# Performance work log

Measured on AMD Instinct MI355X. Metric: run time of the kernel, lower is better.

## Reference

```python
import jax, jax.numpy as jnp
import numpy as np

B, S, D, H = 2, 2048, 1024, 16  # batch, seq, rep_dim, num_heads
DH = D // H
MASK_VALUE = -1e-06  # value passed by MHAttention to masked_softmax (NOT -1e6)


def setup_inputs() -> dict:
    key = jax.random.key(0)
    ks = jax.random.split(key, 16)
    def xavier(k, shape):
        fan_in, fan_out = shape[0], shape[1]
        limit = float(np.sqrt(6.0 / (fan_in + fan_out)))
        return jax.random.uniform(k, shape, jnp.float32, -limit, limit)
    return {
        "queries": jax.random.normal(ks[0], (B, S, D), jnp.float32),
        "keys": jax.random.normal(ks[1], (B, S, D), jnp.float32),
        "values": jax.random.normal(ks[2], (B, S, D), jnp.float32),
        "thresholds": jax.random.randint(ks[3], (B,), 1, S + 1, jnp.int32),
        # Linear params stored as (in, out) so y = x @ W + b
        "Wq": xavier(ks[4], (D, D)), "bq": jnp.zeros((D,), jnp.float32),
        "Wk": xavier(ks[5], (D, D)), "bk": jnp.zeros((D,), jnp.float32),
        "Wv": xavier(ks[6], (D, D)), "bv": jnp.zeros((D,), jnp.float32),
        "W": xavier(ks[7], (DH, DH)),  # learnable bilinear attention matrix
        "Wo": xavier(ks[8], (D, D)), "bo": jnp.zeros((D,), jnp.float32),
    }


def reference(queries, keys, values, thresholds, Wq, bq, Wk, bk, Wv, bv, W, Wo, bo):
    def split_heads(x):  # (B,S,D) -> (B,H,S,DH)
        return x.reshape(B, S, H, DH).transpose(0, 2, 1, 3)

    Q = split_heads(queries @ Wq + bq)
    K = split_heads(keys @ Wk + bk)
    V = split_heads(values @ Wv + bv)

    # bilinear scores: (Q @ W) @ K^T, no 1/sqrt(d) scaling in original
    scores = jnp.einsum("bhqd,bhkd->bhqk", Q @ W, K)
    # mask key positions >= threshold[b] with MASK_VALUE before softmax
    keep = jnp.arange(S)[None, None, None, :] < thresholds[:, None, None, None]
    scores = jnp.where(keep, scores, MASK_VALUE)
    attn = jax.nn.softmax(scores, axis=-1)

    out = jnp.einsum("bhqk,bhkd->bhqd", attn, V)
    out = out.transpose(0, 2, 1, 3).reshape(B, S, D)  # merge heads
    return out @ Wo + bo
```

## Files before the change

### kernel.cpp

```cpp
#include <hip/hip_runtime.h>
#include <hip/hip_bf16.h>

#define D_MODEL 1024
#define NHEADS  16
#define DH      64
#define SEQ     2048
#define BATCH   2

#define LOG2E 1.4426950408889634f
#define MASKB2 (-1e-6f * LOG2E)
#define DEFER_THR 11.5456f
#define NEG_INF (-__builtin_inff())

typedef __attribute__((ext_vector_type(8))) short short8;
typedef __attribute__((ext_vector_type(4))) short short4v;
typedef __attribute__((ext_vector_type(4))) float f32x4;

#define AS1C(p) ((const __attribute__((address_space(1))) void*)(p))
#define AS3(p)  ((__attribute__((address_space(3))) void*)(p))

union PB { short4v s4; unsigned int u[2]; };

static __device__ __forceinline__ float fexp2(float x) {
    return __builtin_amdgcn_exp2f(x);
}

static __device__ __forceinline__ unsigned int pk2(float lo, float hi) {
    __hip_bfloat16 a = __float2bfloat16(lo), b = __float2bfloat16(hi);
    unsigned short au = *(unsigned short*)&a, bu = *(unsigned short*)&b;
    return (unsigned int)au | ((unsigned int)bu << 16);
}

__global__ __launch_bounds__(256) void fold_kernel(const float* __restrict__ Wq,
                                                   const float* __restrict__ bq,
                                                   const float* __restrict__ W,
                                                   float* __restrict__ Wq2,
                                                   float* __restrict__ bq2) {
    if (blockIdx.x < 4096) {
        int idx = blockIdx.x * 256 + threadIdx.x;
        int row = idx >> 10;
        int col = idx & 1023;
        int h = col >> 6, j = col & 63;
        const float* wqr = Wq + (size_t)row * D_MODEL + h * DH;
        float s = 0.f;
#pragma unroll
        for (int d = 0; d < DH; ++d) s += wqr[d] * W[d * DH + j];
        Wq2[idx] = s * LOG2E;
    } else {
        int col = (blockIdx.x - 4096) * 256 + threadIdx.x;
        int h = col >> 6, j = col & 63;
        float s = 0.f;
#pragma unroll
        for (int d = 0; d < DH; ++d) s += bq[h * DH + d] * W[d * DH + j];
        bq2[col] = s * LOG2E;
    }
}

__global__ __launch_bounds__(256) void convert3_kernel(const float* __restrict__ q,
                                                       const float* __restrict__ k,
                                                       const float* __restrict__ v,
                                                       __hip_bfloat16* __restrict__ oq,
                                                       __hip_bfloat16* __restrict__ ok,
                                                       __hip_bfloat16* __restrict__ ov) {
    int z = blockIdx.x >> 11;
    int i = (blockIdx.x & 2047) * 256 + threadIdx.x;
    const float* in = (z == 0) ? q : (z == 1) ? k : v;
    __hip_bfloat16* out = (z == 0) ? oq : (z == 1) ? ok : ov;
    float4 a = *(const float4*)(in + (size_t)i * 8);
    float4 b = *(const float4*)(in + (size_t)i * 8 + 4);
    __hip_bfloat16 o[8];
    o[0] = __float2bfloat16(a.x); o[1] = __float2bfloat16(a.y);
    o[2] = __float2bfloat16(a.z); o[3] = __float2bfloat16(a.w);
    o[4] = __float2bfloat16(b.x); o[5] = __float2bfloat16(b.y);
    o[6] = __float2bfloat16(b.z); o[7] = __float2bfloat16(b.w);
    *(short8*)(out + (size_t)i * 8) = *(short8*)o;
}

__global__ __launch_bounds__(256) void transpose4_kernel(const float* __restrict__ W0,
                                                         const float* __restrict__ W1,
                                                         const float* __restrict__ W2,
                                                         const float* __restrict__ W3,
                                                         __hip_bfloat16* __restrict__ T0,
                                                         __hip_bfloat16* __restrict__ T1,
                                                         __hip_bfloat16* __restrict__ T2,
                                                         __hip_bfloat16* __restrict__ T3) {
    __shared__ float sT[32][33];
    int z = blockIdx.z;
    const float* Win = (z == 0) ? W0 : (z == 1) ? W1 : (z == 2) ? W2 : W3;
    __hip_bfloat16* Wt = (z == 0) ? T0 : (z == 1) ? T1 : (z == 2) ? T2 : T3;
    int n0 = blockIdx.x * 32, k0 = blockIdx.y * 32;
    int tx = threadIdx.x & 31, ty = threadIdx.x >> 5;
#pragma unroll
    for (int i = 0; i < 4; ++i)
        sT[ty + i * 8][tx] = Win[(size_t)(k0 + ty + i * 8) * D_MODEL + n0 + tx];
    __syncthreads();
#pragma unroll
    for (int i = 0; i < 4; ++i)
        Wt[(size_t)(n0 + ty + i * 8) * D_MODEL + k0 + tx] = __float2bfloat16(sT[tx][ty + i * 8]);
}

#define GEMM_CORE(A_, BT_)                                                                  \
    __shared__ __hip_bfloat16 sA[2][128 * 32];                                              \
    __shared__ __hip_bfloat16 sB[2][128 * 32];                                              \
    const int t = threadIdx.x;                                                              \
    const int lane = t & 63, w = t >> 6;                                                    \
    const int g = lane >> 4, li = lane & 15;                                                \
    const int r0 = blockIdx.y * 128, c0 = blockIdx.x * 128;                                 \
    const int wr = (w >> 1) * 64, wc = (w & 1) * 64;                                        \
    f32x4 acc[4][4] = {};                                                                   \
    auto stage = [&](int bb, int k0) {                                                      \
        _Pragma("unroll")                                                                   \
        for (int i = 0; i < 2; ++i) {                                                       \
            int o = (i * 4 + w) * 1024 + lane * 16;                                         \
            int row = o >> 6, ce = (o & 63) >> 1;                                           \
            __builtin_amdgcn_global_load_lds(AS1C(A_ + (size_t)(r0 + row) * 1024 + k0 + ce),\
                                             AS3((char*)sA[bb] + (i * 4 + w) * 1024), 16, 0, 0); \
            __builtin_amdgcn_global_load_lds(AS1C(BT_ + (size_t)(c0 + row) * 1024 + k0 + ce),\
                                             AS3((char*)sB[bb] + (i * 4 + w) * 1024), 16, 0, 0); \
        }                                                                                   \
    };                                                                                      \
    stage(0, 0);                                                                            \
    asm volatile("s_waitcnt vmcnt(0)" ::: "memory");                                        \
    __syncthreads();                                                                        \
    int cur = 0;                                                                            \
    for (int k0 = 0; k0 < 1024; k0 += 32) {                                                 \
        if (k0 + 32 < 1024) stage(cur ^ 1, k0 + 32);                                        \
        short8 af[4], bf[4];                                                                \
        _Pragma("unroll")                                                                   \
        for (int m = 0; m < 4; ++m)                                                         \
            af[m] = *(const short8*)(sA[cur] + (wr + m * 16 + li) * 32 + g * 8);            \
        _Pragma("unroll")                                                                   \
        for (int n = 0; n < 4; ++n)                                                         \
            bf[n] = *(const short8*)(sB[cur] + (wc + n * 16 + li) * 32 + g * 8);            \
        _Pragma("unroll")                                                                   \
        for (int m = 0; m < 4; ++m)                                                         \
            _Pragma("unroll")                                                               \
            for (int n = 0; n < 4; ++n)                                                     \
                acc[m][n] = __builtin_amdgcn_mfma_f32_16x16x32_bf16(af[m], bf[n], acc[m][n], 0, 0, 0); \
        asm volatile("s_waitcnt vmcnt(0)" ::: "memory");                                    \
        __syncthreads();                                                                    \
        cur ^= 1;                                                                           \
    }

__global__ __launch_bounds__(256) void gemm_qkv_kernel(
    const __hip_bfloat16* __restrict__ Xq, const __hip_bfloat16* __restrict__ Xk,
    const __hip_bfloat16* __restrict__ Xv,
    const __hip_bfloat16* __restrict__ WqT, const __hip_bfloat16* __restrict__ WkT,
    const __hip_bfloat16* __restrict__ WvT,
    const float* __restrict__ bq2, const float* __restrict__ bk, const float* __restrict__ bv,
    __hip_bfloat16* __restrict__ Qp, __hip_bfloat16* __restrict__ Kp,
    __hip_bfloat16* __restrict__ Vt) {
    const int z = blockIdx.z;
    const __hip_bfloat16* A  = (z == 0) ? Xq  : (z == 1) ? Xk  : Xv;
    const __hip_bfloat16* BT = (z == 0) ? WqT : (z == 1) ? WkT : WvT;
    const float* bias        = (z == 0) ? bq2 : (z == 1) ? bk  : bv;
    __hip_bfloat16* C        = (z == 0) ? Qp  : (z == 1) ? Kp  : Vt;

    GEMM_CORE(A, BT)

#pragma unroll
    for (int m = 0; m < 4; ++m) {
#pragma unroll
        for (int n = 0; n < 4; ++n) {
            int col = c0 + wc + n * 16 + li;
            float bs = bias[col];
            int row0 = r0 + wr + m * 16 + g * 4;
            int h = col >> 6, d = col & 63;
            if (z == 2) {
                int b = row0 >> 11, s0 = row0 & 2047;
                __hip_bfloat16 o4[4];
#pragma unroll
                for (int r = 0; r < 4; ++r) o4[r] = __float2bfloat16(acc[m][n][r] + bs);
                *(short4*)(C + (((size_t)(b * NHEADS + h)) * DH + d) * SEQ + s0) = *(short4*)o4;
            } else {
#pragma unroll
                for (int r = 0; r < 4; ++r) {
                    int row = row0 + r;
                    int b = row >> 11, s = row & 2047;
                    C[(((size_t)(b * NHEADS + h)) * SEQ + s) * DH + d] =
                        __float2bfloat16(acc[m][n][r] + bs);
                }
            }
        }
    }
}

__global__ __launch_bounds__(256) void gemm_out_kernel(
    const __hip_bfloat16* __restrict__ A, const __hip_bfloat16* __restrict__ BT,
    const float* __restrict__ bias, float* __restrict__ C) {
    GEMM_CORE(A, BT)
#pragma unroll
    for (int m = 0; m < 4; ++m) {
#pragma unroll
        for (int n = 0; n < 4; ++n) {
            int col = c0 + wc + n * 16 + li;
            float bs = bias[col];
            int row0 = r0 + wr + m * 16 + g * 4;
#pragma unroll
            for (int r = 0; r < 4; ++r)
                C[(size_t)(row0 + r) * D_MODEL + col] = acc[m][n][r] + bs;
        }
    }
}

__global__ __launch_bounds__(256) void vsum_kernel(const __hip_bfloat16* __restrict__ Vt,
                                                   const int* __restrict__ thresholds,
                                                   float* __restrict__ Vsum) {
    int bh = blockIdx.x, b = bh >> 4;
    int thresh = thresholds[b];
    int loop_end = min(SEQ, ((thresh + 63) >> 6) << 6);
    int t = threadIdx.x;
    int dh = t >> 2, sub = t & 3;
    const __hip_bfloat16* row = Vt + ((size_t)bh * DH + dh) * SEQ;
    float s = 0.f;
    for (int s0 = loop_end + sub * 8; s0 < SEQ; s0 += 32) {
        short8 v = *(const short8*)(row + s0);
#pragma unroll
        for (int j = 0; j < 8; ++j) {
            unsigned short us = (unsigned short)v[j];
            s += __bfloat162float(*(__hip_bfloat16*)&us);
        }
    }
    s += __shfl_xor(s, 1);
    s += __shfl_xor(s, 2);
    if (sub == 0) Vsum[bh * DH + dh] = s;
}

__global__ __launch_bounds__(256) void attn_mfma_kernel(
    const __hip_bfloat16* __restrict__ Qp,
    const __hip_bfloat16* __restrict__ Kp,
    const __hip_bfloat16* __restrict__ Vt,
    const int* __restrict__ thresholds,
    const float* __restrict__ Vsum,
    __hip_bfloat16* __restrict__ AO) {
    __shared__ char lds[32768];
    char* sK  = lds;
    char* sVT = lds + 16384;

    const int t = threadIdx.x, lane = t & 63, w = t >> 6;
    const int g = lane >> 4, li = lane & 15;
    const int bh = blockIdx.x, b = bh >> 4, h = bh & 15;
    const int q0 = blockIdx.y * 64;
    const int thresh = thresholds[b];
    const int loop_end = min(SEQ, ((thresh + 63) >> 6) << 6);
    const __hip_bfloat16* Qb = Qp + (size_t)bh * SEQ * DH;
    const __hip_bfloat16* Kb = Kp + (size_t)bh * SEQ * DH;
    const __hip_bfloat16* Vb = Vt + (size_t)bh * DH * SEQ;

    short8 qf[2];
#pragma unroll
    for (int kb = 0; kb < 2; ++kb)
        qf[kb] = *(const short8*)(Qb + (size_t)(q0 + w * 16 + li) * DH + kb * 32 + g * 8);

    f32x4 Oacc[4] = {};
    float mrun = NEG_INF, lrun = 0.f;

    auto stageK = [&](int bb, int kv) {
#pragma unroll
        for (int i = 0; i < 2; ++i) {
            int o = i * 4096 + w * 1024 + lane * 16;
            int key = o >> 7, slot = (o & 127) >> 4;
            __builtin_amdgcn_global_load_lds(
                AS1C(Kb + (size_t)(kv + key) * DH + ((slot ^ (key & 7)) << 3)),
                AS3(sK + bb * 8192 + i * 4096 + w * 1024), 16, 0, 0);
        }
    };
    auto stageV = [&](int bb, int kv) {
#pragma unroll
        for (int i = 0; i < 2; ++i) {
            int o = i * 4096 + w * 1024 + lane * 16;
            int dh = o >> 7, slot = (o & 127) >> 4;
            __builtin_amdgcn_global_load_lds(
                AS1C(Vb + (size_t)dh * SEQ + kv + ((slot ^ (dh & 7)) << 3)),
                AS3(sVT + bb * 8192 + i * 4096 + w * 1024), 16, 0, 0);
        }
    };

    stageK(0, 0); stageV(0, 0);
    asm volatile("s_waitcnt vmcnt(0)" ::: "memory");
    __syncthreads();

    int cur = 0;
    for (int kv0 = 0; kv0 < loop_end; kv0 += 64) {
        int nxt = kv0 + 64;
        if (nxt < loop_end) { stageK(cur ^ 1, nxt); stageV(cur ^ 1, nxt); }

        f32x4 S[4] = {};
        __builtin_amdgcn_s_setprio(1);
#pragma unroll
        for (int kb = 0; kb < 2; ++kb) {
            short8 kf[4];
#pragma unroll
            for (int n = 0; n < 4; ++n) {
                int key = 16 * n + li;
                kf[n] = *(const short8*)(sK + cur * 8192 + key * 128 +
                                         (((4 * kb + g) ^ (key & 7)) << 4));
            }
#pragma unroll
            for (int n = 0; n < 4; ++n)
                S[n] = __builtin_amdgcn_mfma_f32_16x16x32_bf16(kf[n], qf[kb], S[n], 0, 0, 0);
        }
        __builtin_amdgcn_s_setprio(0);

        if (kv0 + 64 > thresh) {
            int tr = thresh - kv0 - 4 * g;
#pragma unroll
            for (int n = 0; n < 4; ++n)
#pragma unroll
                for (int rr = 0; rr < 4; ++rr)
                    if (16 * n + rr >= tr) S[n][rr] = MASKB2;
        }

        float mx = S[0][0];
#pragma unroll
        for (int n = 0; n < 4; ++n)
#pragma unroll
            for (int rr = 0; rr < 4; ++rr) mx = fmaxf(mx, S[n][rr]);
        mx = fmaxf(mx, __shfl_xor(mx, 16));
        mx = fmaxf(mx, __shfl_xor(mx, 32));
        float pmax = mx;

        if (__any(pmax > mrun + DEFER_THR)) {
            float mn = fmaxf(mrun, pmax);
            float alpha = fexp2(mrun - mn);
            lrun *= alpha;
#pragma unroll
            for (int n = 0; n < 4; ++n)
#pragma unroll
                for (int rr = 0; rr < 4; ++rr) Oacc[n][rr] *= alpha;
            mrun = mn;
        }

        short4v pb[4];
        float rs = 0.f;
#pragma unroll
        for (int n = 0; n < 4; ++n) {
#pragma unroll
            for (int rr = 0; rr < 4; ++rr) {
                float p = fexp2(S[n][rr] - mrun);
                S[n][rr] = p;
                rs += p;
            }
            PB u;
            u.u[0] = pk2(S[n][0], S[n][1]);
            u.u[1] = pk2(S[n][2], S[n][3]);
            pb[n] = u.s4;
        }
        rs += __shfl_xor(rs, 16);
        rs += __shfl_xor(rs, 32);
        lrun += rs;

        __builtin_amdgcn_s_setprio(1);
#pragma unroll
        for (int ks = 0; ks < 4; ++ks) {
            int slot = 2 * ks + (g >> 1);
            int sub8 = 8 * (g & 1);
#pragma unroll
            for (int n = 0; n < 4; ++n) {
                int dh = 16 * n + li;
                short4v va = *(const short4v*)(sVT + cur * 8192 + dh * 128 +
                                               ((slot ^ (dh & 7)) << 4) + sub8);
                Oacc[n] = __builtin_amdgcn_mfma_f32_16x16x16bf16_1k(va, pb[ks], Oacc[n], 0, 0, 0);
            }
        }
        __builtin_amdgcn_s_setprio(0);

        asm volatile("s_waitcnt vmcnt(0)" ::: "memory");
        __syncthreads();
        cur ^= 1;
    }

    int nmask = SEQ - loop_end;
    if (nmask > 0) {
        const float* vs = Vsum + bh * DH;
        f32x4 vsf[4];
#pragma unroll
        for (int n = 0; n < 4; ++n) vsf[n] = *(const f32x4*)(vs + 16 * n + 4 * g);
        float pu = fexp2(MASKB2 - mrun);
        lrun += (float)nmask * pu;
#pragma unroll
        for (int n = 0; n < 4; ++n)
#pragma unroll
            for (int rr = 0; rr < 4; ++rr) Oacc[n][rr] += pu * vsf[n][rr];
    }

    float linv = 1.0f / lrun;
    int q = q0 + w * 16 + li;
#pragma unroll
    for (int n = 0; n < 4; ++n) {
        __hip_bfloat16 o4[4];
#pragma unroll
        for (int rr = 0; rr < 4; ++rr) o4[rr] = __float2bfloat16(Oacc[n][rr] * linv);
        *(short4*)(AO + (size_t)(b * SEQ + q) * D_MODEL + h * DH + 16 * n + 4 * g) =
            *(short4*)o4;
    }
}

extern "C" void kernel_launch(void* const* d_in, const int* in_sizes, int n_in,
                              void* d_out, int out_size, void* d_ws, size_t ws_size,
                              hipStream_t stream) {
    const float* queries    = (const float*)d_in[0];
    const float* keys       = (const float*)d_in[1];
    const float* values     = (const float*)d_in[2];
    const int*   thresholds = (const int*)d_in[3];
    const float* Wq = (const float*)d_in[4];
    const float* bq = (const float*)d_in[5];
    const float* Wk = (const float*)d_in[6];
    const float* bk = (const float*)d_in[7];
    const float* Wv = (const float*)d_in[8];
    const float* bv = (const float*)d_in[9];
    const float* W  = (const float*)d_in[10];
    const float* Wo = (const float*)d_in[11];
    const float* bo = (const float*)d_in[12];
    float* out = (float*)d_out;

    char* wsb = (char*)d_ws;
    float* bq2  = (float*)wsb;
    float* Vsum = (float*)(wsb + 4096);
    float* Wq2  = (float*)(wsb + 16384);
    __hip_bfloat16* XqB = (__hip_bfloat16*)(wsb + 16384 + (4 << 20));
    __hip_bfloat16* XkB = XqB + (1 << 22);
    __hip_bfloat16* XvB = XkB + (1 << 22);
    __hip_bfloat16* WqT = XvB + (1 << 22);
    __hip_bfloat16* WkT = WqT + (1 << 20);
    __hip_bfloat16* WvT = WkT + (1 << 20);
    __hip_bfloat16* WoT = WvT + (1 << 20);
    __hip_bfloat16* QpB = WoT + (1 << 20);
    __hip_bfloat16* KpB = QpB + (1 << 22);
    __hip_bfloat16* VtB = KpB + (1 << 22);
    __hip_bfloat16* AOB = XqB;

    fold_kernel<<<4100, 256, 0, stream>>>(Wq, bq, W, Wq2, bq2);
    convert3_kernel<<<6144, 256, 0, stream>>>(queries, keys, values, XqB, XkB, XvB);
    transpose4_kernel<<<dim3(32, 32, 4), 256, 0, stream>>>(Wq2, Wk, Wv, Wo,
                                                           WqT, WkT, WvT, WoT);

    gemm_qkv_kernel<<<dim3(8, 32, 3), 256, 0, stream>>>(XqB, XkB, XvB, WqT, WkT, WvT,
                                                        bq2, bk, bv, QpB, KpB, VtB);
    vsum_kernel<<<32, 256, 0, stream>>>(VtB, thresholds, Vsum);

    attn_mfma_kernel<<<dim3(32, 32), 256, 0, stream>>>(QpB, KpB, VtB, thresholds, Vsum, AOB);

    gemm_out_kernel<<<dim3(8, 32), 256, 0, stream>>>(AOB, WoT, bo, out);
}
```

Baseline: 174.0 us.

## Fuse fp32-to-bf16 input conversion into QKV GEMM and software-pipeline attention

Removes the separate convert kernel. The QKV GEMM now loads fp32 activations directly into swizzled LDS and packs them to bf16 in registers, which saves a full write/read round trip of the converted inputs. The attention loop is also restructured into a two-stage software pipeline: the QK^T MFMAs and V fragment loads for tile t+1 are issued before the softmax and PV for tile t, so the two phases can overlap. The cost is twice the LDS for the A tile, extra conversion work inside the GEMM loop, and higher register pressure in attention from the doubled S and V register sets.

New measurement: 248.6 us. 42.9% more time.

```diff
diff --git a/kernel.cpp b/kernel.cpp
--- a/kernel.cpp
+++ b/kernel.cpp
@@ -19,7 +19,8 @@
 #define AS1C(p) ((const __attribute__((address_space(1))) void*)(p))
 #define AS3(p)  ((__attribute__((address_space(3))) void*)(p))
 
-union PB { short4v s4; unsigned int u[2]; };
+union PB  { short4v s4; unsigned int u[2]; };
+union PW8 { short8  s8; unsigned int u[4]; };
 
 static __device__ __forceinline__ float fexp2(float x) {
     return __builtin_amdgcn_exp2f(x);
@@ -54,26 +55,6 @@
         for (int d = 0; d < DH; ++d) s += bq[h * DH + d] * W[d * DH + j];
         bq2[col] = s * LOG2E;
     }
-}
-
-__global__ __launch_bounds__(256) void convert3_kernel(const float* __restrict__ q,
-                                                       const float* __restrict__ k,
-                                                       const float* __restrict__ v,
-                                                       __hip_bfloat16* __restrict__ oq,
-                                                       __hip_bfloat16* __restrict__ ok,
-                                                       __hip_bfloat16* __restrict__ ov) {
-    int z = blockIdx.x >> 11;
-    int i = (blockIdx.x & 2047) * 256 + threadIdx.x;
-    const float* in = (z == 0) ? q : (z == 1) ? k : v;
-    __hip_bfloat16* out = (z == 0) ? oq : (z == 1) ? ok : ov;
-    float4 a = *(const float4*)(in + (size_t)i * 8);
-    float4 b = *(const float4*)(in + (size_t)i * 8 + 4);
-    __hip_bfloat16 o[8];
-    o[0] = __float2bfloat16(a.x); o[1] = __float2bfloat16(a.y);
-    o[2] = __float2bfloat16(a.z); o[3] = __float2bfloat16(a.w);
-    o[4] = __float2bfloat16(b.x); o[5] = __float2bfloat16(b.y);
-    o[6] = __float2bfloat16(b.z); o[7] = __float2bfloat16(b.w);
-    *(short8*)(out + (size_t)i * 8) = *(short8*)o;
 }
 
 __global__ __launch_bounds__(256) void transpose4_kernel(const float* __restrict__ W0,
@@ -98,6 +79,66 @@
     for (int i = 0; i < 4; ++i)
         Wt[(size_t)(n0 + ty + i * 8) * D_MODEL + k0 + tx] = __float2bfloat16(sT[tx][ty + i * 8]);
 }
+
+#define GEMM_CORE_F32A(A_, BT_)                                                             \
+    __shared__ float sAf[2][128 * 32];                                                      \
+    __shared__ __hip_bfloat16 sB[2][128 * 32];                                              \
+    const int t = threadIdx.x;                                                              \
+    const int lane = t & 63, w = t >> 6;                                                    \
+    const int g = lane >> 4, li = lane & 15;                                                \
+    const int r0 = blockIdx.y * 128, c0 = blockIdx.x * 128;                                 \
+    const int wr = (w >> 1) * 64, wc = (w & 1) * 64;                                        \
+    f32x4 acc[4][4] = {};                                                                   \
+    auto stage = [&](int bb, int k0) {                                                      \
+        _Pragma("unroll")                                                                   \
+        for (int i = 0; i < 4; ++i) {                                                       \
+            int o = (i * 4 + w) * 1024 + lane * 16;              \
+            int row = o >> 7;                                                \
+            int slot = (o & 127) >> 4;                                                      \
+            int sslot = slot ^ (row & 7);                    \
+            __builtin_amdgcn_global_load_lds(                                               \
+                AS1C(A_ + (size_t)(r0 + row) * 1024 + k0 + sslot * 4),                      \
+                AS3((char*)sAf[bb] + (i * 4 + w) * 1024), 16, 0, 0);                        \
+        }                                                                                   \
+        _Pragma("unroll")                                                                   \
+        for (int i = 0; i < 2; ++i) {                                                       \
+            int o = (i * 4 + w) * 1024 + lane * 16;                                         \
+            int row = o >> 6, ce = (o & 63) >> 1;                                           \
+            __builtin_amdgcn_global_load_lds(AS1C(BT_ + (size_t)(c0 + row) * 1024 + k0 + ce),\
+                                             AS3((char*)sB[bb] + (i * 4 + w) * 1024), 16, 0, 0); \
+        }                                                                                   \
+    };                                                                                      \
+    stage(0, 0);                                                                            \
+    asm volatile("s_waitcnt vmcnt(0)" ::: "memory");                                        \
+    __syncthreads();                                                                        \
+    const int xr0 = (((2 * g)     ^ (li & 7)) << 4);                                        \
+    const int xr1 = (((2 * g + 1) ^ (li & 7)) << 4);                                        \
+    int cur = 0;                                                                            \
+    for (int k0 = 0; k0 < 1024; k0 += 32) {                                                 \
+        if (k0 + 32 < 1024) stage(cur ^ 1, k0 + 32);                                        \
+        short8 af[4], bf[4];                                                                \
+        _Pragma("unroll")                                                                   \
+        for (int m = 0; m < 4; ++m) {                                                       \
+            const char* base = (const char*)sAf[cur] + (wr + m * 16 + li) * 128;            \
+            f32x4 a0 = *(const f32x4*)(base + xr0);                                         \
+            f32x4 a1 = *(const f32x4*)(base + xr1);                                         \
+            PW8 uu;                                                                         \
+            uu.u[0] = pk2(a0[0], a0[1]); uu.u[1] = pk2(a0[2], a0[3]);                       \
+            uu.u[2] = pk2(a1[0], a1[1]); uu.u[3] = pk2(a1[2], a1[3]);                       \
+            af[m] = uu.s8;                                                                  \
+        }                                                                                   \
+        _Pragma("unroll")                                                                   \
+        for (int n = 0; n < 4; ++n)                                                         \
+            bf[n] = *(const short8*)(sB[cur] + (wc + n * 16 + li) * 32 + g * 8);            \
+        _Pragma("unroll")                                                                   \
+        for (int m = 0; m < 4; ++m)                                                         \
+            _Pragma("unroll")                                                               \
+            for (int n = 0; n < 4; ++n)                                                     \
+                acc[m][n] = __builtin_amdgcn_mfma_f32_16x16x32_bf16(af[m], bf[n], acc[m][n], 0, 0, 0); \
+        asm volatile("s_waitcnt vmcnt(0)" ::: "memory");                                    \
+        __syncthreads();                                                                    \
+        cur ^= 1;                                                                           \
+    }
 
 #define GEMM_CORE(A_, BT_)                                                                  \
     __shared__ __hip_bfloat16 sA[2][128 * 32];                                              \
@@ -143,20 +184,19 @@
     }
 
 __global__ __launch_bounds__(256) void gemm_qkv_kernel(
-    const __hip_bfloat16* __restrict__ Xq, const __hip_bfloat16* __restrict__ Xk,
-    const __hip_bfloat16* __restrict__ Xv,
+    const float* __restrict__ Xq, const float* __restrict__ Xk, const float* __restrict__ Xv,
     const __hip_bfloat16* __restrict__ WqT, const __hip_bfloat16* __restrict__ WkT,
     const __hip_bfloat16* __restrict__ WvT,
     const float* __restrict__ bq2, const float* __restrict__ bk, const float* __restrict__ bv,
     __hip_bfloat16* __restrict__ Qp, __hip_bfloat16* __restrict__ Kp,
     __hip_bfloat16* __restrict__ Vt) {
     const int z = blockIdx.z;
-    const __hip_bfloat16* A  = (z == 0) ? Xq  : (z == 1) ? Xk  : Xv;
+    const float* A           = (z == 0) ? Xq  : (z == 1) ? Xk  : Xv;
     const __hip_bfloat16* BT = (z == 0) ? WqT : (z == 1) ? WkT : WvT;
     const float* bias        = (z == 0) ? bq2 : (z == 1) ? bk  : bv;
     __hip_bfloat16* C        = (z == 0) ? Qp  : (z == 1) ? Kp  : Vt;
 
-    GEMM_CORE(A, BT)
+    GEMM_CORE_F32A(A, BT)
 
 #pragma unroll
     for (int m = 0; m < 4; ++m) {
@@ -243,6 +283,7 @@
     const int q0 = blockIdx.y * 64;
     const int thresh = thresholds[b];
     const int loop_end = min(SEQ, ((thresh + 63) >> 6) << 6);
+    const int nt = loop_end >> 6;
     const __hip_bfloat16* Qb = Qp + (size_t)bh * SEQ * DH;
     const __hip_bfloat16* Kb = Kp + (size_t)bh * SEQ * DH;
     const __hip_bfloat16* Vb = Vt + (size_t)bh * DH * SEQ;
@@ -276,99 +317,144 @@
         }
     };
 
+    f32x4 S_e[4], S_o[4];
+    short4v V_e[16], V_o[16];
+
+#define QK_TILE(SS, kbase, kv0_)                                                           \
+    {                                                                                      \
+        _Pragma("unroll")                                                                  \
+        for (int n = 0; n < 4; ++n) {                                                      \
+            SS[n][0] = 0.f; SS[n][1] = 0.f; SS[n][2] = 0.f; SS[n][3] = 0.f;                \
+        }                                                                                  \
+        __builtin_amdgcn_s_setprio(1);                                                     \
+        _Pragma("unroll")                                                                  \
+        for (int kb = 0; kb < 2; ++kb) {                                                   \
+            short8 kf[4];                                                                  \
+            _Pragma("unroll")                                                              \
+            for (int n = 0; n < 4; ++n) {                                                  \
+                int key = 16 * n + li;                                                     \
+                kf[n] = *(const short8*)((kbase) + key * 128 +                             \
+                                         (((4 * kb + g) ^ (key & 7)) << 4));               \
+            }                                                                              \
+            _Pragma("unroll")                                                              \
+            for (int n = 0; n < 4; ++n)                                                    \
+                SS[n] = __builtin_amdgcn_mfma_f32_16x16x32_bf16(kf[n], qf[kb], SS[n], 0, 0, 0); \
+        }                                                                                  \
+        __builtin_amdgcn_s_setprio(0);                                                     \
+        if ((kv0_) + 64 > thresh) {                                                        \
+            int tr = thresh - (kv0_) - 4 * g;                                              \
+            _Pragma("unroll")                                                              \
+            for (int n = 0; n < 4; ++n)                                                    \
+                _Pragma("unroll")                                                          \
+                for (int rr = 0; rr < 4; ++rr)                                             \
+                    if (16 * n + rr >= tr) SS[n][rr] = MASKB2;                             \
+        }                                                                                  \
+    }
+
+#define VLOAD(VR, vbase)                                                                   \
+    {                                                                                      \
+        _Pragma("unroll")                                                                  \
+        for (int ks = 0; ks < 4; ++ks) {                                                   \
+            int slot = 2 * ks + (g >> 1);                                                  \
+            _Pragma("unroll")                                                              \
+            for (int n = 0; n < 4; ++n) {                                                  \
+                int dh = 16 * n + li;                                                      \
+                VR[4 * ks + n] = *(const short4v*)((vbase) + dh * 128 +                    \
+                                  ((slot ^ (dh & 7)) << 4) + 8 * (g & 1));                 \
+            }                                                                              \
+        }                                                                                  \
+    }
+
+#define SMPV(SP, VP)                                                                       \
+    {                                                                                      \
+        float mx = SP[0][0];                                                               \
+        _Pragma("unroll")                                                                  \
+        for (int n = 0; n < 4; ++n)                                                        \
+            _Pragma("unroll")                                                              \
+            for (int rr = 0; rr < 4; ++rr) mx = fmaxf(mx, SP[n][rr]);                      \
+        mx = fmaxf(mx, __shfl_xor(mx, 16));                                                \
+        mx = fmaxf(mx, __shfl_xor(mx, 32));                                                \
+        if (__any(mx > mrun + DEFER_THR)) {                                                \
+            float mn = fmaxf(mrun, mx);                                                    \
+            float alpha = fexp2(mrun - mn);                                                \
+            lrun *= alpha;                                                                 \
+            _Pragma("unroll")                                                              \
+            for (int n = 0; n < 4; ++n)                                                    \
+                _Pragma("unroll")                                                          \
+                for (int rr = 0; rr < 4; ++rr) Oacc[n][rr] *= alpha;                       \
+            mrun = mn;                                                                     \
+        }                                                                                  \
+        short4v pb[4];                                                                     \
+        float rs = 0.f;                                                                    \
+        _Pragma("unroll")                                                                  \
+        for (int n = 0; n < 4; ++n) {                                                      \
+            _Pragma("unroll")                                                              \
+            for (int rr = 0; rr < 4; ++rr) {                                               \
+                float p = fexp2(SP[n][rr] - mrun);                                         \
+                SP[n][rr] = p;                                                             \
+                rs += p;                                                                   \
+            }                                                                              \
+            PB u;                                                                          \
+            u.u[0] = pk2(SP[n][0], SP[n][1]);                                              \
+            u.u[1] = pk2(SP[n][2], SP[n][3]);                                              \
+            pb[n] = u.s4;                                                                  \
+        }                                                                                  \
+        rs += __shfl_xor(rs, 16);                                                          \
+        rs += __shfl_xor(rs, 32);                                                          \
+        lrun += rs;                                                                        \
+        __builtin_amdgcn_s_setprio(1);                                                     \
+        _Pragma("unroll")                                                                  \
+        for (int ks = 0; ks < 4; ++ks)                                                     \
+            _Pragma("unroll")                                                              \
+            for (int n = 0; n < 4; ++n)                                                    \
+                Oacc[n] = __builtin_amdgcn_mfma_f32_16x16x16bf16_1k(VP[4 * ks + n], pb[ks],\
+                                                                    Oacc[n], 0, 0, 0);     \
+        __builtin_amdgcn_s_setprio(0);                                                     \
+    }
+
     stageK(0, 0); stageV(0, 0);
     asm volatile("s_waitcnt vmcnt(0)" ::: "memory");
     __syncthreads();
 
-    int cur = 0;
-    for (int kv0 = 0; kv0 < loop_end; kv0 += 64) {
-        int nxt = kv0 + 64;
-        if (nxt < loop_end) { stageK(cur ^ 1, nxt); stageV(cur ^ 1, nxt); }
-
-        f32x4 S[4] = {};
-        __builtin_amdgcn_s_setprio(1);
-#pragma unroll
-        for (int kb = 0; kb < 2; ++kb) {
-            short8 kf[4];
-#pragma unroll
-            for (int n = 0; n < 4; ++n) {
-                int key = 16 * n + li;
-                kf[n] = *(const short8*)(sK + cur * 8192 + key * 128 +
-                                         (((4 * kb + g) ^ (key & 7)) << 4));
-            }
-#pragma unroll
-            for (int n = 0; n < 4; ++n)
-                S[n] = __builtin_amdgcn_mfma_f32_16x16x32_bf16(kf[n], qf[kb], S[n], 0, 0, 0);
-        }
-        __builtin_amdgcn_s_setprio(0);
-
-        if (kv0 + 64 > thresh) {
-            int tr = thresh - kv0 - 4 * g;
-#pragma unroll
-            for (int n = 0; n < 4; ++n)
-#pragma unroll
-                for (int rr = 0; rr < 4; ++rr)
-                    if (16 * n + rr >= tr) S[n][rr] = MASKB2;
-        }
-
-        float mx = S[0][0];
-#pragma unroll
-        for (int n = 0; n < 4; ++n)
-#pragma unroll
-            for (int rr = 0; rr < 4; ++rr) mx = fmaxf(mx, S[n][rr]);
-        mx = fmaxf(mx, __shfl_xor(mx, 16));
-        mx = fmaxf(mx, __shfl_xor(mx, 32));
-        float pmax = mx;
-
-        if (__any(pmax > mrun + DEFER_THR)) {
-            float mn = fmaxf(mrun, pmax);
-            float alpha = fexp2(mrun - mn);
-            lrun *= alpha;
-#pragma unroll
-            for (int n = 0; n < 4; ++n)
-#pragma unroll
-                for (int rr = 0; rr < 4; ++rr) Oacc[n][rr] *= alpha;
-            mrun = mn;
-        }
-
-        short4v pb[4];
-        float rs = 0.f;
-#pragma unroll
-        for (int n = 0; n < 4; ++n) {
-#pragma unroll
-            for (int rr = 0; rr < 4; ++rr) {
-                float p = fexp2(S[n][rr] - mrun);
-                S[n][rr] = p;
-                rs += p;
-            }
-            PB u;
-            u.u[0] = pk2(S[n][0], S[n][1]);
-            u.u[1] = pk2(S[n][2], S[n][3]);
-            pb[n] = u.s4;
-        }
-        rs += __shfl_xor(rs, 16);
-        rs += __shfl_xor(rs, 32);
-        lrun += rs;
-
-        __builtin_amdgcn_s_setprio(1);
-#pragma unroll
-        for (int ks = 0; ks < 4; ++ks) {
-            int slot = 2 * ks + (g >> 1);
-            int sub8 = 8 * (g & 1);
-#pragma unroll
-            for (int n = 0; n < 4; ++n) {
-                int dh = 16 * n + li;
-                short4v va = *(const short4v*)(sVT + cur * 8192 + dh * 128 +
-                                               ((slot ^ (dh & 7)) << 4) + sub8);
-                Oacc[n] = __builtin_amdgcn_mfma_f32_16x16x16bf16_1k(va, pb[ks], Oacc[n], 0, 0, 0);
-            }
-        }
-        __builtin_amdgcn_s_setprio(0);
-
+    if (nt > 1) { stageK(1, 64); stageV(1, 64); }
+    QK_TILE(S_e, sK, 0);
+    VLOAD(V_e, sVT);
+    if (nt > 1) {
         asm volatile("s_waitcnt vmcnt(0)" ::: "memory");
         __syncthreads();
-        cur ^= 1;
-    }
+    }
+
+    int tt = 1;
+    while (tt < nt) {
+        {
+            int kv0 = tt << 6;
+            if (tt + 1 < nt) { stageK(0, kv0 + 64); stageV(0, kv0 + 64); }
+            QK_TILE(S_o, sK + 8192, kv0);
+            VLOAD(V_o, sVT + 8192);
+            SMPV(S_e, V_e);
+            if (tt + 1 < nt) {
+                asm volatile("s_waitcnt vmcnt(0)" ::: "memory");
+                __syncthreads();
+            }
+        }
+        ++tt;
+        if (tt >= nt) break;
+        {
+            int kv0 = tt << 6;
+            if (tt + 1 < nt) { stageK(1, kv0 + 64); stageV(1, kv0 + 64); }
+            QK_TILE(S_e, sK, kv0);
+            VLOAD(V_e, sVT);
+            SMPV(S_o, V_o);
+            if (tt + 1 < nt) {
+                asm volatile("s_waitcnt vmcnt(0)" ::: "memory");
+                __syncthreads();
+            }
+        }
+        ++tt;
+    }
+
+    if (nt & 1) { SMPV(S_e, V_e); }
+    else        { SMPV(S_o, V_o); }
 
     int nmask = SEQ - loop_end;
     if (nmask > 0) {
@@ -394,6 +480,9 @@
         *(short4*)(AO + (size_t)(b * SEQ + q) * D_MODEL + h * DH + 16 * n + 4 * g) =
             *(short4*)o4;
     }
+#undef QK_TILE
+#undef VLOAD
+#undef SMPV
 }
 
 extern "C" void kernel_launch(void* const* d_in, const int* in_sizes, int n_in,
@@ -418,24 +507,21 @@
     float* bq2  = (float*)wsb;
     float* Vsum = (float*)(wsb + 4096);
     float* Wq2  = (float*)(wsb + 16384);
-    __hip_bfloat16* XqB = (__hip_bfloat16*)(wsb + 16384 + (4 << 20));
-    __hip_bfloat16* XkB = XqB + (1 << 22);
-    __hip_bfloat16* XvB = XkB + (1 << 22);
-    __hip_bfloat16* WqT = XvB + (1 << 22);
+    __hip_bfloat16* WqT = (__hip_bfloat16*)(wsb + 16384 + (4 << 20));
     __hip_bfloat16* WkT = WqT + (1 << 20);
     __hip_bfloat16* WvT = WkT + (1 << 20);
     __hip_bfloat16* WoT = WvT + (1 << 20);
     __hip_bfloat16* QpB = WoT + (1 << 20);
     __hip_bfloat16* KpB = QpB + (1 << 22);
     __hip_bfloat16* VtB = KpB + (1 << 22);
-    __hip_bfloat16* AOB = XqB;
+    __hip_bfloat16* AOB = VtB + (1 << 22);
 
     fold_kernel<<<4100, 256, 0, stream>>>(Wq, bq, W, Wq2, bq2);
-    convert3_kernel<<<6144, 256, 0, stream>>>(queries, keys, values, XqB, XkB, XvB);
     transpose4_kernel<<<dim3(32, 32, 4), 256, 0, stream>>>(Wq2, Wk, Wv, Wo,
                                                            WqT, WkT, WvT, WoT);
 
-    gemm_qkv_kernel<<<dim3(8, 32, 3), 256, 0, stream>>>(XqB, XkB, XvB, WqT, WkT, WvT,
+    gemm_qkv_kernel<<<dim3(8, 32, 3), 256, 0, stream>>>(queries, keys, values,
+                                                        WqT, WkT, WvT,
                                                         bq2, bk, bv, QpB, KpB, VtB);
     vsum_kernel<<<32, 256, 0, stream>>>(VtB, thresholds, Vsum);
 
```
